# Performance work log

Measured on AMD Instinct MI355X. Metric: run time of the kernel, lower is better.

## Reference

```python
import jax, jax.numpy as jnp
import numpy as np

NEG_SLOPE = 0.2
BN_EPS = 1e-5

def gat_conv(x, src, dst, W, a_src, a_dst, bias, heads, out_ch):
    """PyG-style GATConv (eval mode, self-loops already in src/dst)."""
    N = x.shape[0]
    h = (x @ W).reshape(N, heads, out_ch)                 # [N,H,C]
    alpha_src = jnp.sum(h * a_src, axis=-1)               # [N,H]
    alpha_dst = jnp.sum(h * a_dst, axis=-1)               # [N,H]
    e = jax.nn.leaky_relu(alpha_src[src] + alpha_dst[dst], NEG_SLOPE)  # [E,H]
    # softmax over edges grouped by destination node
    m = jax.ops.segment_max(e, dst, num_segments=N)
    e = jnp.exp(e - m[dst])
    denom = jax.ops.segment_sum(e, dst, num_segments=N)
    alpha = e / (denom[dst] + 1e-16)                      # [E,H]
    msg = h[src] * alpha[:, :, None]                      # [E,H,C]
    out = jax.ops.segment_sum(msg, dst, num_segments=N)   # [N,H,C]
    return out.reshape(N, heads * out_ch) + bias

def bn_inf(x, gamma, beta, mean, var):
    return (x - mean) * jax.lax.rsqrt(var + BN_EPS) * gamma + beta

def setup_inputs() -> dict:
    key = jax.random.key(0)
    ks = iter(jax.random.split(key, 64))
    N, E, G = 50000, 800000, 256
    IN, H, HEADS, OUT = 58, 64, 4, 128
    D = H * HEADS  # 256
    inp = {}
    inp['x'] = jax.random.normal(next(ks), (N, IN), dtype=jnp.float32)
    inp['edge_index'] = jax.random.randint(next(ks), (2, E), 0, N)
    inp['batch'] = jnp.sort(jax.random.randint(next(ks), (N,), 0, G))
    inp['global_features'] = jax.random.normal(next(ks), (G, 7), dtype=jnp.float32)
    def lin(k, fi, fo):
        return jax.random.normal(k, (fi, fo), dtype=jnp.float32) / np.sqrt(fi)
    dims = [(IN, H, HEADS), (D, H, HEADS), (D, H, HEADS), (D, OUT, 1)]
    for i, (fi, c, hd) in enumerate(dims, 1):
        inp[f'W{i}'] = lin(next(ks), fi, hd * c)
        inp[f'a{i}s'] = jax.random.normal(next(ks), (hd, c), dtype=jnp.float32) / np.sqrt(c)
        inp[f'a{i}d'] = jax.random.normal(next(ks), (hd, c), dtype=jnp.float32) / np.sqrt(c)
        inp[f'b{i}'] = jnp.zeros((hd * c,), dtype=jnp.float32)
        bd = hd * c
        inp[f'g{i}'] = jnp.ones((bd,), dtype=jnp.float32)
        inp[f'be{i}'] = jnp.zeros((bd,), dtype=jnp.float32)
        inp[f'm{i}'] = 0.1 * jax.random.normal(next(ks), (bd,), dtype=jnp.float32)
        inp[f'v{i}'] = jax.random.uniform(next(ks), (bd,), dtype=jnp.float32) + 0.5
    inp['pw1'] = lin(next(ks), OUT, 32); inp['pb1'] = jnp.zeros((32,), jnp.float32)
    inp['pw2'] = lin(next(ks), 32, 1);   inp['pb2'] = jnp.zeros((1,), jnp.float32)
    inp['gw'] = lin(next(ks), 7, 32);    inp['gb'] = jnp.zeros((32,), jnp.float32)
    return inp

def reference(x, edge_index, batch, global_features,
              W1, a1s, a1d, b1, g1, be1, m1, v1,
              W2, a2s, a2d, b2, g2, be2, m2, v2,
              W3, a3s, a3d, b3, g3, be3, m3, v3,
              W4, a4s, a4d, b4, g4, be4, m4, v4,
              pw1, pb1, pw2, pb2, gw, gb):
    N = x.shape[0]
    G = global_features.shape[0]
    loops = jnp.arange(N)
    src = jnp.concatenate([edge_index[0], loops])  # add self-loops (PyG default)
    dst = jnp.concatenate([edge_index[1], loops])
    x1 = jax.nn.relu(bn_inf(gat_conv(x,  src, dst, W1, a1s, a1d, b1, 4, 64), g1, be1, m1, v1))
    x2 = jax.nn.relu(bn_inf(gat_conv(x1, src, dst, W2, a2s, a2d, b2, 4, 64), g2, be2, m2, v2))
    x3 = jax.nn.relu(bn_inf(gat_conv(x1 + x2, src, dst, W3, a3s, a3d, b3, 4, 64), g3, be3, m3, v3))
    x4 = jax.nn.relu(bn_inf(gat_conv(x3, src, dst, W4, a4s, a4d, b4, 1, 128), g4, be4, m4, v4))
    # GlobalAttention pooling: gate -> per-graph softmax -> weighted sum
    gate = jax.nn.relu(x4 @ pw1 + pb1) @ pw2 + pb2        # [N,1]
    gm = jax.ops.segment_max(gate, batch, num_segments=G)
    ge = jnp.exp(gate - gm[batch])
    gden = jax.ops.segment_sum(ge, batch, num_segments=G)
    attn = ge / (gden[batch] + 1e-16)                     # [N,1]
    emb = jax.ops.segment_sum(attn * x4, batch, num_segments=G)  # [G,128]
    gf = jax.nn.relu(global_features @ gw + gb)           # [G,32] (dropout off in eval)
    return jnp.concatenate([emb, gf], axis=-1)            # [G,160]
```

## Files before the change

kernel.cpp:

```cpp
#include <hip/hip_runtime.h>
#include <cstdint>
#include <cstddef>

#define NEG_SLOPE 0.2f
#define BN_EPS 1e-5f

typedef __bf16 bf16x8 __attribute__((ext_vector_type(8)));
typedef float  f32x4  __attribute__((ext_vector_type(4)));

__device__ __forceinline__ float ub0(unsigned u) { return (float)(u & 0xffu); }
__device__ __forceinline__ float ub1(unsigned u) { return (float)((u >> 8) & 0xffu); }
__device__ __forceinline__ float ub2(unsigned u) { return (float)((u >> 16) & 0xffu); }
__device__ __forceinline__ float ub3(unsigned u) { return (float)((u >> 24) & 0xffu); }

__global__ void conv_pad_kernel(const float* __restrict__ x, __bf16* __restrict__ xb,
                                int N, int K) {
    int i = blockIdx.x * blockDim.x + threadIdx.x;
    int total = N * 8;
    for (; i < total; i += gridDim.x * blockDim.x) {
        int n = i >> 3, p = i & 7;
        bf16x8 v;
        #pragma unroll
        for (int j = 0; j < 8; ++j) {
            int k = p * 8 + j;
            v[j] = (k < K) ? (__bf16)x[(size_t)n * K + k] : (__bf16)0.f;
        }
        *(bf16x8*)&xb[((size_t)p * N + n) * 8] = v;
    }
}

__global__ void prep_all_kernel(
    const float* __restrict__ W1, const float* __restrict__ W2,
    const float* __restrict__ W3, const float* __restrict__ W4,
    const float* __restrict__ PW1,
    __bf16* __restrict__ wt1, __bf16* __restrict__ wt2,
    __bf16* __restrict__ wt3, __bf16* __restrict__ wt4,
    __bf16* __restrict__ pw1t,
    const float* b1, const float* g1, const float* e1, const float* m1, const float* v1,
    const float* b2, const float* g2, const float* e2, const float* m2, const float* v2,
    const float* b3, const float* g3, const float* e3, const float* m3, const float* v3,
    const float* b4, const float* g4, const float* e4, const float* m4, const float* v4,
    float* __restrict__ bnS, float* __restrict__ bnT,
    int IN) {
    int b = blockIdx.x;
    if (b >= 928) {
        int l = b - 928;
        int Dl = (l == 3) ? 128 : 256;
        int t = threadIdx.x;
        if (t < Dl) {
            const float* bias; const float* ga; const float* be;
            const float* mu;   const float* va;
            if (l == 0)      { bias = b1; ga = g1; be = e1; mu = m1; va = v1; }
            else if (l == 1) { bias = b2; ga = g2; be = e2; mu = m2; va = v2; }
            else if (l == 2) { bias = b3; ga = g3; be = e3; mu = m3; va = v3; }
            else             { bias = b4; ga = g4; be = e4; mu = m4; va = v4; }
            float S = ga[t] * rsqrtf(va[t] + BN_EPS);
            bnS[l * 256 + t] = S;
            bnT[l * 256 + t] = (bias[t] - mu[t]) * S + be[t];
        }
        return;
    }
    const float* W; __bf16* WT; int K, D, Kpad, col; bool panel = true;
    if (b < 256)      { W = W1;  WT = wt1;  K = IN;  D = 256; Kpad = 64;  col = b; }
    else if (b < 512) { W = W2;  WT = wt2;  K = 256; D = 256; Kpad = 256; col = b - 256; }
    else if (b < 768) { W = W3;  WT = wt3;  K = 256; D = 256; Kpad = 256; col = b - 512; }
    else if (b < 896) { W = W4;  WT = wt4;  K = 256; D = 128; Kpad = 256; col = b - 768; }
    else              { W = PW1; WT = pw1t; K = 128; D = 32;  Kpad = 128; col = b - 896; panel = false; }
    for (int k = threadIdx.x; k < Kpad; k += blockDim.x) {
        float v = (k < K) ? W[(size_t)k * D + col] : 0.f;
        if (panel)
            WT[((size_t)(k >> 3) * D + col) * 8 + (k & 7)] = (__bf16)v;
        else
            WT[(size_t)col * Kpad + k] = (__bf16)v;
    }
}

template<int DCOLS, int KT, bool HAS_A2>
__global__ __launch_bounds__(256) void gemm_fused(
    const __bf16* __restrict__ A, const __bf16* __restrict__ A2,
    const __bf16* __restrict__ WT,
    const float* __restrict__ asv, const float* __restrict__ adv,
    uint8_t* __restrict__ H8, float* __restrict__ hscale,
    float* __restrict__ alpha_s, float* __restrict__ alpha_d,
    int M) {
    constexpr int NSB = DCOLS / 64;
    constexpr int RB  = (DCOLS == 256) ? 32 : 64;
    const int w    = threadIdx.x >> 6;
    const int lane = threadIdx.x & 63;
    const int l16  = lane & 15, hi4 = lane >> 4;
    const int rbase = (DCOLS == 256) ? 0 : (w >> 1) * 32;
    const int ct    = (DCOLS == 256) ? w : (w & 1);
    const int col0w = ct * 64;
    const int n0 = blockIdx.x * RB;

    f32x4 acc[2][4] = {};
    int arow[2];
    #pragma unroll
    for (int i = 0; i < 2; ++i) {
        int r = n0 + rbase + i * 16 + l16;
        arow[i] = (r < M) ? r : (M - 1);
    }

    #pragma unroll
    for (int k0 = 0; k0 < KT; k0 += 32) {
        const int panel = (k0 >> 3) + hi4;
        bf16x8 af[2], bfr[4];
        #pragma unroll
        for (int i = 0; i < 2; ++i) {
            bf16x8 v = *(const bf16x8*)&A[((size_t)panel * M + arow[i]) * 8];
            if (HAS_A2) {
                bf16x8 v2 = *(const bf16x8*)&A2[((size_t)panel * M + arow[i]) * 8];
                #pragma unroll
                for (int j = 0; j < 8; ++j) v[j] = (__bf16)((float)v[j] + (float)v2[j]);
            }
            af[i] = v;
        }
        #pragma unroll
        for (int j = 0; j < 4; ++j)
            bfr[j] = *(const bf16x8*)&WT[((size_t)panel * DCOLS + col0w + j * 16 + l16) * 8];
        #pragma unroll
        for (int i = 0; i < 2; ++i)
            #pragma unroll
            for (int j = 0; j < 4; ++j)
                acc[i][j] = __builtin_amdgcn_mfma_f32_16x16x32_bf16(
                    af[i], bfr[j], acc[i][j], 0, 0, 0);
    }

    float asc[4], adc[4];
    #pragma unroll
    for (int j = 0; j < 4; ++j) {
        int c = col0w + j * 16 + l16;
        asc[j] = asv[c]; adc[j] = adv[c];
    }
    __shared__ float as_l[(DCOLS == 128) ? 64 : 1][2], ad_l[(DCOLS == 128) ? 64 : 1][2];
    #pragma unroll
    for (int i = 0; i < 2; ++i)
        #pragma unroll
        for (int q = 0; q < 4; ++q) {
            float ps = 0.f, pd = 0.f;
            #pragma unroll
            for (int j = 0; j < 4; ++j) {
                float v = acc[i][j][q];
                ps = fmaf(v, asc[j], ps);
                pd = fmaf(v, adc[j], pd);
            }
            #pragma unroll
            for (int o = 1; o < 16; o <<= 1) {
                ps += __shfl_xor(ps, o, 64);
                pd += __shfl_xor(pd, o, 64);
            }
            int rl = rbase + i * 16 + hi4 * 4 + q;
            if constexpr (DCOLS == 256) {
                int row = n0 + rl;
                if (l16 == 0 && row < M) {
                    alpha_s[row * 4 + w] = ps;
                    alpha_d[row * 4 + w] = pd;
                }
            } else {
                if (l16 == 0) { as_l[rl][ct] = ps; ad_l[rl][ct] = pd; }
            }
        }
    if constexpr (DCOLS == 128) {
        __syncthreads();
        int t = threadIdx.x;
        if (t < 64) {
            int row = n0 + t;
            if (row < M) {
                alpha_s[row] = as_l[t][0] + as_l[t][1];
                alpha_d[row] = ad_l[t][0] + ad_l[t][1];
            }
        }
    }

    #pragma unroll
    for (int i = 0; i < 2; ++i)
        #pragma unroll
        for (int q = 0; q < 4; ++q) {
            float m = fabsf(acc[i][0][q]);
            #pragma unroll
            for (int j = 1; j < 4; ++j) m = fmaxf(m, fabsf(acc[i][j][q]));
            #pragma unroll
            for (int o = 1; o < 16; o <<= 1) m = fmaxf(m, __shfl_xor(m, o, 64));
            float qinv = (m > 1e-30f) ? 127.f / m : 0.f;
            int row = n0 + rbase + i * 16 + hi4 * 4 + q;
            if (row < M) {
                if (l16 == 0) hscale[row * NSB + ct] = m * (1.f / 127.f);
                #pragma unroll
                for (int j = 0; j < 4; ++j)
                    H8[(size_t)row * DCOLS + col0w + j * 16 + l16] =
                        (uint8_t)((int)rintf(acc[i][j][q] * qinv) + 128);
            }
        }
}

__global__ void deg_count_kernel(const int* __restrict__ ei, int* __restrict__ deg,
                                 int E, int Etot) {
    int e = blockIdx.x * blockDim.x + threadIdx.x;
    if (e >= Etot) return;
    int d = (e < E) ? ei[E + e] : e - E;
    atomicAdd(&deg[d], 1);
}

#define SCB 4096
__global__ __launch_bounds__(256) void scan1_kernel(const int* __restrict__ deg,
                                                    int* __restrict__ bsum, int N) {
    __shared__ int ts[256];
    const int t = threadIdx.x;
    const int base = blockIdx.x * SCB + t * 16;
    int s = 0;
    #pragma unroll
    for (int i = 0; i < 16; ++i) {
        int idx = base + i;
        if (idx < N) s += deg[idx];
    }
    ts[t] = s;
    __syncthreads();
    for (int off = 128; off > 0; off >>= 1) {
        if (t < off) ts[t] += ts[t + off];
        __syncthreads();
    }
    if (t == 0) bsum[blockIdx.x] = ts[0];
}

__global__ __launch_bounds__(256) void scan2_kernel(const int* __restrict__ bsum,
                                                    int* __restrict__ bpref, int B,
                                                    int* __restrict__ rowptrN) {
    __shared__ int sm[256];
    const int t = threadIdx.x;
    int v = (t < B) ? bsum[t] : 0;
    sm[t] = v;
    __syncthreads();
    for (int off = 1; off < 256; off <<= 1) {
        int u = (t >= off) ? sm[t - off] : 0;
        __syncthreads();
        sm[t] += u;
        __syncthreads();
    }
    if (t < B) bpref[t] = sm[t] - v;
    if (t == 255) *rowptrN = sm[255];
}

__global__ __launch_bounds__(256) void scan3_kernel(const int* __restrict__ deg,
                                                    const int* __restrict__ bpref,
                                                    int* __restrict__ rowptr,
                                                    int* __restrict__ cursor, int N) {
    __shared__ int ts[256];
    const int t = threadIdx.x;
    const int base = blockIdx.x * SCB + t * 16;
    int d[16];
    int s = 0;
    #pragma unroll
    for (int i = 0; i < 16; ++i) {
        int idx = base + i;
        d[i] = (idx < N) ? deg[idx] : 0;
        s += d[i];
    }
    ts[t] = s;
    __syncthreads();
    for (int off = 1; off < 256; off <<= 1) {
        int u = (t >= off) ? ts[t - off] : 0;
        __syncthreads();
        ts[t] += u;
        __syncthreads();
    }
    int run = bpref[blockIdx.x] + ts[t] - s;
    #pragma unroll
    for (int i = 0; i < 16; ++i) {
        int idx = base + i;
        if (idx < N) { rowptr[idx] = run; cursor[idx] = run; run += d[i]; }
    }
}

__global__ void scatter_kernel(const int* __restrict__ ei, int* __restrict__ cursor,
                               int* __restrict__ csrc, int E, int Etot) {
    int e = blockIdx.x * blockDim.x + threadIdx.x;
    if (e >= Etot) return;
    int s, d;
    if (e < E) { s = ei[e]; d = ei[E + e]; } else { s = d = e - E; }
    int pos = atomicAdd(&cursor[d], 1);
    csrc[pos] = s;
}

__global__ void gstart_kernel(const int* __restrict__ batch, int* __restrict__ gstart,
                              int N, int G) {
    int n = blockIdx.x * blockDim.x + threadIdx.x;
    if (n >= N) return;
    int b = batch[n];
    if (n == 0) { for (int g = 0; g <= b; ++g) gstart[g] = 0; }
    else {
        int bp = batch[n - 1];
        for (int g = bp + 1; g <= b; ++g) gstart[g] = n;
    }
    if (n == N - 1) { for (int g = b + 1; g <= G; ++g) gstart[g] = N; }
}

template<int HEADS, int C, bool OUTP>
__global__ __launch_bounds__(256) void gat_agg(
    const int* __restrict__ rowptr, const int* __restrict__ csrc,
    const uint8_t* __restrict__ hf, const float* __restrict__ hscale,
    const float* __restrict__ asrc, const float* __restrict__ adst,
    const float* __restrict__ bnS, const float* __restrict__ bnT,
    __bf16* __restrict__ out, int N) {
    constexpr int D   = HEADS * C;
    constexpr int NSB = D / 64;
    constexpr int LPE = D / 8;
    constexpr int EPH = 32 / LPE;

    const int wid  = threadIdx.x >> 6;
    const int lane = threadIdx.x & 63;
    const int half = lane >> 5;
    const int sl   = lane & 31;

    __shared__ int   soff[4][2][32];
    __shared__ float pal[4][2][32][NSB];

    const int npairs = (N + 1) >> 1;

    for (int pair = blockIdx.x * 4 + wid; pair < npairs; pair += gridDim.x * 4) {
        const int node = pair * 2 + half;
        const bool valid = node < N;
        const int beg = valid ? rowptr[node] : 0;
        const int end = valid ? rowptr[node + 1] : 0;
        const int deg = end - beg;

        const int grp = (EPH == 1) ? 0 : (sl >> 4);
        const int c0  = (EPH == 1) ? sl * 8 : (sl & 15) * 8;
        const int sb  = c0 >> 6;
        const uint8_t* hb = hf + c0;

        float ad[HEADS];
        #pragma unroll
        for (int h = 0; h < HEADS; ++h) ad[h] = valid ? adst[node * HEADS + h] : 0.f;

        float acc8[8] = {};
        float psum = 0.f;

        auto fmau8 = [&](uint2 v, float q) {
            acc8[0] = fmaf(ub0(v.x), q, acc8[0]);
            acc8[1] = fmaf(ub1(v.x), q, acc8[1]);
            acc8[2] = fmaf(ub2(v.x), q, acc8[2]);
            acc8[3] = fmaf(ub3(v.x), q, acc8[3]);
            acc8[4] = fmaf(ub0(v.y), q, acc8[4]);
            acc8[5] = fmaf(ub1(v.y), q, acc8[5]);
            acc8[6] = fmaf(ub2(v.y), q, acc8[6]);
            acc8[7] = fmaf(ub3(v.y), q, acc8[7]);
        };

        auto agg_chunk = [&](int cnt) {
            const int steps = (cnt + 8 * EPH - 1) / (8 * EPH);
            for (int s = 0; s < steps; ++s) {
                const int e = s * 8 * EPH;
                int o[8]; float q[8]; uint2 v[8];
                #pragma unroll
                for (int u = 0; u < 8; ++u) {
                    o[u] = soff[wid][half][e + u * EPH + grp];
                    q[u] = pal[wid][half][e + u * EPH + grp][sb];
                }
                #pragma unroll
                for (int u = 0; u < 8; ++u) v[u] = *(const uint2*)(hb + o[u]);
                #pragma unroll
                for (int u = 0; u < 8; ++u) { psum += q[u]; fmau8(v[u], q[u]); }
            }
        };

        if (deg <= 32) {
            const bool act = sl < deg;
            int msrc = act ? csrc[beg + sl] : 0;
            float lv[HEADS];
            if constexpr (HEADS == 4) {
                float4 a4 = ((const float4*)asrc)[msrc];
                lv[0] = a4.x; lv[1] = a4.y; lv[2] = a4.z; lv[3] = a4.w;
            } else {
                lv[0] = asrc[msrc];
            }
            float pe_[HEADS];
            #pragma unroll
            for (int h = 0; h < HEADS; ++h) {
                float v;
                if (act) { v = lv[h] + ad[h]; v = v > 0.f ? v : NEG_SLOPE * v; }
                else v = -INFINITY;
                float mx = v;
                #pragma unroll
                for (int o = 1; o < 32; o <<= 1) mx = fmaxf(mx, __shfl_xor(mx, o, 64));
                float pe = act ? __expf(v - mx) : 0.f;
                float ps = pe;
                #pragma unroll
                for (int o = 1; o < 32; o <<= 1) ps += __shfl_xor(ps, o, 64);
                pe_[h] = pe * (1.f / (ps + 1e-16f));
            }
            soff[wid][half][sl] = msrc * D;
            if constexpr (HEADS == 4) {
                float4 hs = act ? ((const float4*)hscale)[msrc]
                                : make_float4(0.f, 0.f, 0.f, 0.f);
                *(float4*)&pal[wid][half][sl][0] =
                    make_float4(pe_[0] * hs.x, pe_[1] * hs.y, pe_[2] * hs.z, pe_[3] * hs.w);
            } else {
                float2 hs = act ? ((const float2*)hscale)[msrc] : make_float2(0.f, 0.f);
                *(float2*)&pal[wid][half][sl][0] = make_float2(pe_[0] * hs.x, pe_[0] * hs.y);
            }
            asm volatile("s_waitcnt lgkmcnt(0)" ::: "memory");
            agg_chunk(deg);
        } else {
            float mx[HEADS], sm[HEADS], inv[HEADS];
            #pragma unroll
            for (int h = 0; h < HEADS; ++h) mx[h] = -INFINITY;
            for (int j = beg + sl; j < end; j += 32) {
                int s = csrc[j];
                #pragma unroll
                for (int h = 0; h < HEADS; ++h) {
                    float v = asrc[s * HEADS + h] + ad[h];
                    v = v > 0.f ? v : NEG_SLOPE * v;
                    mx[h] = fmaxf(mx[h], v);
                }
            }
            #pragma unroll
            for (int h = 0; h < HEADS; ++h) {
                #pragma unroll
                for (int o = 1; o < 32; o <<= 1) mx[h] = fmaxf(mx[h], __shfl_xor(mx[h], o, 64));
                sm[h] = 0.f;
            }
            for (int j = beg + sl; j < end; j += 32) {
                int s = csrc[j];
                #pragma unroll
                for (int h = 0; h < HEADS; ++h) {
                    float v = asrc[s * HEADS + h] + ad[h];
                    v = v > 0.f ? v : NEG_SLOPE * v;
                    sm[h] += __expf(v - mx[h]);
                }
            }
            #pragma unroll
            for (int h = 0; h < HEADS; ++h) {
                #pragma unroll
                for (int o = 1; o < 32; o <<= 1) sm[h] += __shfl_xor(sm[h], o, 64);
                inv[h] = 1.f / (sm[h] + 1e-16f);
            }
            for (int base2 = beg; base2 < end; base2 += 32) {
                int ne = min(32, end - base2);
                bool act2 = sl < ne;
                int msrc = csrc[base2 + (act2 ? sl : 0)];
                soff[wid][half][sl] = msrc * D;
                if constexpr (HEADS == 4) {
                    float4 hs = act2 ? ((const float4*)hscale)[msrc]
                                     : make_float4(0.f, 0.f, 0.f, 0.f);
                    float hsv[4] = {hs.x, hs.y, hs.z, hs.w};
                    #pragma unroll
                    for (int h = 0; h < 4; ++h) {
                        float pv = 0.f;
                        if (act2) {
                            float v = asrc[msrc * 4 + h] + ad[h];
                            v = v > 0.f ? v : NEG_SLOPE * v;
                            pv = __expf(v - mx[h]) * inv[h];
                        }
                        pal[wid][half][sl][h] = pv * hsv[h];
                    }
                } else {
                    float2 hs = act2 ? ((const float2*)hscale)[msrc] : make_float2(0.f, 0.f);
                    float pv = 0.f;
                    if (act2) {
                        float v = asrc[msrc] + ad[0];
                        v = v > 0.f ? v : NEG_SLOPE * v;
                        pv = __expf(v - mx[0]) * inv[0];
                    }
                    pal[wid][half][sl][0] = pv * hs.x;
                    pal[wid][half][sl][1] = pv * hs.y;
                }
                asm volatile("s_waitcnt lgkmcnt(0)" ::: "memory");
                agg_chunk(ne);
                asm volatile("s_waitcnt lgkmcnt(0)" ::: "memory");
            }
        }

        if constexpr (EPH == 2) {
            #pragma unroll
            for (int i = 0; i < 8; ++i)
                acc8[i] += __shfl_xor(acc8[i], 16, 64);
            psum += __shfl_xor(psum, 16, 64);
        }

        if (valid && (EPH == 1 || sl < 16)) {
            float4 Sa = *(const float4*)&bnS[c0];
            float4 Sb = *(const float4*)&bnS[c0 + 4];
            float4 Ta = *(const float4*)&bnT[c0];
            float4 Tb = *(const float4*)&bnT[c0 + 4];
            float S8[8] = {Sa.x, Sa.y, Sa.z, Sa.w, Sb.x, Sb.y, Sb.z, Sb.w};
            float T8[8] = {Ta.x, Ta.y, Ta.z, Ta.w, Tb.x, Tb.y, Tb.z, Tb.w};
            bf16x8 ov;
            #pragma unroll
            for (int i = 0; i < 8; ++i) {
                float v = fmaf(acc8[i] - 128.f * psum, S8[i], T8[i]);
                ov[i] = (__bf16)fmaxf(v, 0.f);
            }
            if constexpr (OUTP)
                *(bf16x8*)&out[((size_t)(c0 >> 3) * N + node) * 8] = ov;
            else
                *(bf16x8*)&out[(size_t)node * D + c0] = ov;
        }
    }
}

__global__ __launch_bounds__(256) void gate_gemm_kernel(
    const __bf16* __restrict__ x4, const __bf16* __restrict__ pw1t,
    const float* __restrict__ pb1, const float* __restrict__ pw2,
    const float* __restrict__ pb2, float* __restrict__ gate, int N) {
    const int w    = threadIdx.x >> 6;
    const int lane = threadIdx.x & 63;
    const int l16  = lane & 15, hi4 = lane >> 4;
    const int n0 = (blockIdx.x * 4 + w) * 16;
    if (n0 >= N) return;
    const int arow = min(n0 + l16, N - 1);
    f32x4 acc[2] = {};
    #pragma unroll
    for (int k0 = 0; k0 < 128; k0 += 32) {
        bf16x8 af = *(const bf16x8*)&x4[(size_t)arow * 128 + k0 + hi4 * 8];
        bf16x8 b0 = *(const bf16x8*)&pw1t[(size_t)l16 * 128 + k0 + hi4 * 8];
        bf16x8 b1 = *(const bf16x8*)&pw1t[(size_t)(16 + l16) * 128 + k0 + hi4 * 8];
        acc[0] = __builtin_amdgcn_mfma_f32_16x16x32_bf16(af, b0, acc[0], 0, 0, 0);
        acc[1] = __builtin_amdgcn_mfma_f32_16x16x32_bf16(af, b1, acc[1], 0, 0, 0);
    }
    float pb1a = pb1[l16], pb1b = pb1[16 + l16];
    float w2a = pw2[l16], w2b = pw2[16 + l16];
    #pragma unroll
    for (int q = 0; q < 4; ++q) {
        float g = fmaxf(acc[0][q] + pb1a, 0.f) * w2a +
                  fmaxf(acc[1][q] + pb1b, 0.f) * w2b;
        #pragma unroll
        for (int o = 1; o < 16; o <<= 1) g += __shfl_xor(g, o, 64);
        int row = n0 + hi4 * 4 + q;
        if (l16 == 0 && row < N) gate[row] = g + pb2[0];
    }
}

__global__ __launch_bounds__(128) void pool_kernel(
    const __bf16* __restrict__ x4, const float* __restrict__ gate,
    const int* __restrict__ gstart, float* __restrict__ out) {
    const int g = blockIdx.x;
    const int t = threadIdx.x;
    const int beg = gstart[g], end = gstart[g + 1];
    __shared__ float red[128];
    __shared__ float wbuf[128];
    float m = -INFINITY;
    for (int n = beg + t; n < end; n += 128) m = fmaxf(m, gate[n]);
    red[t] = m; __syncthreads();
    for (int off = 64; off > 0; off >>= 1) {
        if (t < off) red[t] = fmaxf(red[t], red[t + off]);
        __syncthreads();
    }
    m = red[0]; __syncthreads();
    float s = 0.f;
    for (int n = beg + t; n < end; n += 128) s += expf(gate[n] - m);
    red[t] = s; __syncthreads();
    for (int off = 64; off > 0; off >>= 1) {
        if (t < off) red[t] += red[t + off];
        __syncthreads();
    }
    const float inv = 1.f / (red[0] + 1e-16f);
    __syncthreads();
    float acc = 0.f;
    for (int base = beg; base < end; base += 128) {
        int ne = min(128, end - base);
        if (t < ne) wbuf[t] = expf(gate[base + t] - m) * inv;
        __syncthreads();
        for (int i = 0; i < ne; ++i)
            acc = fmaf(wbuf[i], (float)x4[(size_t)(base + i) * 128 + t], acc);
        __syncthreads();
    }
    out[(size_t)g * 160 + t] = acc;
}

__global__ void gfeat_kernel(const float* __restrict__ gfeat,
                             const float* __restrict__ gw, const float* __restrict__ gb,
                             float* __restrict__ out) {
    const int g = blockIdx.x;
    const int k = threadIdx.x;
    if (k < 32) {
        float t = gb[k];
        #pragma unroll
        for (int j = 0; j < 7; ++j) t = fmaf(gfeat[g * 7 + j], gw[j * 32 + k], t);
        out[(size_t)g * 160 + 128 + k] = fmaxf(t, 0.f);
    }
}

extern "C" void kernel_launch(void* const* d_in, const int* in_sizes, int n_in,
                              void* d_out, int out_size, void* d_ws, size_t ws_size,
                              hipStream_t stream) {
    const float* x      = (const float*)d_in[0];
    const int*   ei     = (const int*)  d_in[1];
    const int*   batch  = (const int*)  d_in[2];
    const float* gfeat  = (const float*)d_in[3];

    const int N    = in_sizes[2];
    const int E    = in_sizes[1] / 2;
    const int G    = in_sizes[3] / 7;
    const int IN   = in_sizes[0] / N;
    const int Etot = E + N;

    const float* W[4];  const float* avs[4]; const float* avd[4]; const float* bi[4];
    const float* ga[4]; const float* be[4];  const float* mu[4];  const float* va[4];
    for (int l = 0; l < 4; ++l) {
        int o = 4 + 8 * l;
        W[l]   = (const float*)d_in[o + 0];
        avs[l] = (const float*)d_in[o + 1];
        avd[l] = (const float*)d_in[o + 2];
        bi[l]  = (const float*)d_in[o + 3];
        ga[l]  = (const float*)d_in[o + 4];
        be[l]  = (const float*)d_in[o + 5];
        mu[l]  = (const float*)d_in[o + 6];
        va[l]  = (const float*)d_in[o + 7];
    }
    const float* pw1 = (const float*)d_in[36];
    const float* pb1 = (const float*)d_in[37];
    const float* pw2 = (const float*)d_in[38];
    const float* pb2 = (const float*)d_in[39];
    const float* gw  = (const float*)d_in[40];
    const float* gb  = (const float*)d_in[41];

    float* out = (float*)d_out;

    float* ws = (float*)d_ws;
    __bf16* xb = (__bf16*)ws; ws += (size_t)N * 32;
    uint8_t* h8 = (uint8_t*)ws; ws += (size_t)N * 64;
    float* hsc = ws;  ws += (size_t)N * 4;
    __bf16* x1 = (__bf16*)ws; ws += (size_t)N * 128;
    __bf16* x2 = (__bf16*)ws; ws += (size_t)N * 128;
    __bf16* x3 = (__bf16*)ws; ws += (size_t)N * 128;
    __bf16* wt1 = (__bf16*)ws; ws += 256 * 64 / 2;
    __bf16* wt2 = (__bf16*)ws; ws += 256 * 256 / 2;
    __bf16* wt3 = (__bf16*)ws; ws += 256 * 256 / 2;
    __bf16* wt4 = (__bf16*)ws; ws += 128 * 256 / 2;
    __bf16* pw1t = (__bf16*)ws; ws += 32 * 128 / 2;
    float* bnS = ws; ws += 4 * 256;
    float* bnT = ws; ws += 4 * 256;
    float* asrc = ws;  ws += (size_t)N * 4;
    float* adst = ws;  ws += (size_t)N * 4;
    float* gate = ws;  ws += N;
    int* deg    = (int*)ws; ws += N;
    int* cursor = (int*)ws; ws += N;
    int* rowptr = (int*)ws; ws += (N + 1);
    int* csrc   = (int*)ws; ws += Etot;
    int* gstart = (int*)ws; ws += (G + 1);
    int* bsum   = (int*)ws; ws += 256;
    int* bpref  = (int*)ws; ws += 256;
    __bf16* x4 = x1;

    const int SB = (N + SCB - 1) / SCB;

    hipLaunchKernelGGL(conv_pad_kernel, dim3(512), dim3(256), 0, stream, x, xb, N, IN);
    hipLaunchKernelGGL(prep_all_kernel, dim3(932), dim3(256), 0, stream,
                       W[0], W[1], W[2], W[3], pw1, wt1, wt2, wt3, wt4, pw1t,
                       bi[0], ga[0], be[0], mu[0], va[0],
                       bi[1], ga[1], be[1], mu[1], va[1],
                       bi[2], ga[2], be[2], mu[2], va[2],
                       bi[3], ga[3], be[3], mu[3], va[3],
                       bnS, bnT, IN);

    hipMemsetAsync(deg, 0, (size_t)N * 4, stream);
    hipLaunchKernelGGL(deg_count_kernel, dim3((Etot + 255) / 256), dim3(256), 0, stream,
                       ei, deg, E, Etot);
    hipLaunchKernelGGL(scan1_kernel, dim3(SB), dim3(256), 0, stream, deg, bsum, N);
    hipLaunchKernelGGL(scan2_kernel, dim3(1), dim3(256), 0, stream, bsum, bpref, SB,
                       &rowptr[N]);
    hipLaunchKernelGGL(scan3_kernel, dim3(SB), dim3(256), 0, stream, deg, bpref,
                       rowptr, cursor, N);
    hipLaunchKernelGGL(scatter_kernel, dim3((Etot + 255) / 256), dim3(256), 0, stream,
                       ei, cursor, csrc, E, Etot);
    hipLaunchKernelGGL(gstart_kernel, dim3((N + 255) / 256), dim3(256), 0, stream,
                       batch, gstart, N, G);

    const int grid32  = (N + 31) / 32;
    const int grid64  = (N + 63) / 64;
    const int gatgrid = 2048;

    hipLaunchKernelGGL((gemm_fused<256, 64, false>), dim3(grid32), dim3(256), 0, stream,
                       xb, nullptr, wt1, avs[0], avd[0], h8, hsc, asrc, adst, N);
    hipLaunchKernelGGL((gat_agg<4, 64, true>), dim3(gatgrid), dim3(256), 0, stream,
                       rowptr, csrc, h8, hsc, asrc, adst, bnS + 0, bnT + 0, x1, N);
    hipLaunchKernelGGL((gemm_fused<256, 256, false>), dim3(grid32), dim3(256), 0, stream,
                       x1, nullptr, wt2, avs[1], avd[1], h8, hsc, asrc, adst, N);
    hipLaunchKernelGGL((gat_agg<4, 64, true>), dim3(gatgrid), dim3(256), 0, stream,
                       rowptr, csrc, h8, hsc, asrc, adst, bnS + 256, bnT + 256, x2, N);
    hipLaunchKernelGGL((gemm_fused<256, 256, true>), dim3(grid32), dim3(256), 0, stream,
                       x1, x2, wt3, avs[2], avd[2], h8, hsc, asrc, adst, N);
    hipLaunchKernelGGL((gat_agg<4, 64, true>), dim3(gatgrid), dim3(256), 0, stream,
                       rowptr, csrc, h8, hsc, asrc, adst, bnS + 512, bnT + 512, x3, N);
    hipLaunchKernelGGL((gemm_fused<128, 256, false>), dim3(grid64), dim3(256), 0, stream,
                       x3, nullptr, wt4, avs[3], avd[3], h8, hsc, asrc, adst, N);
    hipLaunchKernelGGL((gat_agg<1, 128, false>), dim3(gatgrid), dim3(256), 0, stream,
                       rowptr, csrc, h8, hsc, asrc, adst, bnS + 768, bnT + 768, x4, N);

    hipLaunchKernelGGL(gate_gemm_kernel, dim3((N + 63) / 64), dim3(256), 0, stream,
                       x4, pw1t, pb1, pw2, pb2, gate, N);
    hipLaunchKernelGGL(pool_kernel, dim3(G), dim3(128), 0, stream, x4, gate, gstart, out);
    hipLaunchKernelGGL(gfeat_kernel, dim3(G), dim3(64), 0, stream, gfeat, gw, gb, out);
}
```

Measured before the change: 410.5 us.

## Build CSR via two-level bucket partition instead of global atomic scatter

Replaces the per-node degree count, three-pass scan and global-atomic scatter with a bucketed counting sort. Edges are first counted and partitioned into buckets of 128 destination nodes using shared-memory atomics, then each bucket is sorted locally in LDS to produce rowptr and csrc. This aims to cut contended global atomics and scattered writes during CSR construction, at the cost of an extra temporary int2 edge buffer and one more pass over the edges. It assumes at most 512 buckets, so N must not exceed 65536.

```diff
diff --git a/kernel.cpp b/kernel.cpp
--- a/kernel.cpp
+++ b/kernel.cpp
@@ -193,92 +193,123 @@
         }
 }
 
-__global__ void deg_count_kernel(const int* __restrict__ ei, int* __restrict__ deg,
-                                 int E, int Etot) {
-    int e = blockIdx.x * blockDim.x + threadIdx.x;
-    if (e >= Etot) return;
-    int d = (e < E) ? ei[E + e] : e - E;
-    atomicAdd(&deg[d], 1);
-}
-
-#define SCB 4096
-__global__ __launch_bounds__(256) void scan1_kernel(const int* __restrict__ deg,
-                                                    int* __restrict__ bsum, int N) {
-    __shared__ int ts[256];
+#define NPB_SHIFT 7
+#define NPB 128
+#define NBMAX 512
+#define P3CH 4096
+#define STAGE 4608
+
+__global__ __launch_bounds__(256) void bcount_kernel(const int* __restrict__ ei,
+                                                     int* __restrict__ bcnt,
+                                                     int E, int Etot) {
+    __shared__ int bc[NBMAX];
+    for (int i = threadIdx.x; i < NBMAX; i += 256) bc[i] = 0;
+    __syncthreads();
+    for (int e = blockIdx.x * blockDim.x + threadIdx.x; e < Etot;
+         e += gridDim.x * blockDim.x) {
+        int d = (e < E) ? ei[E + e] : e - E;
+        atomicAdd(&bc[d >> NPB_SHIFT], 1);
+    }
+    __syncthreads();
+    for (int i = threadIdx.x; i < NBMAX; i += 256)
+        if (bc[i]) atomicAdd(&bcnt[i], bc[i]);
+}
+
+__global__ __launch_bounds__(512) void bscan_kernel(const int* __restrict__ bcnt,
+                                                    int* __restrict__ bbase,
+                                                    int* __restrict__ bcursor,
+                                                    int* __restrict__ rowptrN, int Etot) {
+    __shared__ int sm[512];
     const int t = threadIdx.x;
-    const int base = blockIdx.x * SCB + t * 16;
-    int s = 0;
-    #pragma unroll
-    for (int i = 0; i < 16; ++i) {
-        int idx = base + i;
-        if (idx < N) s += deg[idx];
-    }
-    ts[t] = s;
-    __syncthreads();
-    for (int off = 128; off > 0; off >>= 1) {
-        if (t < off) ts[t] += ts[t + off];
-        __syncthreads();
-    }
-    if (t == 0) bsum[blockIdx.x] = ts[0];
-}
-
-__global__ __launch_bounds__(256) void scan2_kernel(const int* __restrict__ bsum,
-                                                    int* __restrict__ bpref, int B,
-                                                    int* __restrict__ rowptrN) {
-    __shared__ int sm[256];
+    int v = bcnt[t];
+    sm[t] = v;
+    __syncthreads();
+    for (int off = 1; off < 512; off <<= 1) {
+        int u = (t >= off) ? sm[t - off] : 0;
+        __syncthreads();
+        sm[t] += u;
+        __syncthreads();
+    }
+    bbase[t] = sm[t] - v;
+    bcursor[t] = sm[t] - v;
+    if (t == 0) *rowptrN = Etot;
+}
+
+__global__ __launch_bounds__(256) void partition_kernel(const int* __restrict__ ei,
+                                                        int* __restrict__ bcursor,
+                                                        int2* __restrict__ tmp,
+                                                        int E, int Etot) {
+    __shared__ int lcnt[NBMAX], gb[NBMAX], lcur[NBMAX];
     const int t = threadIdx.x;
-    int v = (t < B) ? bsum[t] : 0;
-    sm[t] = v;
-    __syncthreads();
-    for (int off = 1; off < 256; off <<= 1) {
-        int u = (t >= off) ? sm[t - off] : 0;
-        __syncthreads();
-        sm[t] += u;
-        __syncthreads();
-    }
-    if (t < B) bpref[t] = sm[t] - v;
-    if (t == 255) *rowptrN = sm[255];
-}
-
-__global__ __launch_bounds__(256) void scan3_kernel(const int* __restrict__ deg,
-                                                    const int* __restrict__ bpref,
-                                                    int* __restrict__ rowptr,
-                                                    int* __restrict__ cursor, int N) {
-    __shared__ int ts[256];
+    const int base = blockIdx.x * P3CH;
+    for (int i = t; i < NBMAX; i += 256) { lcnt[i] = 0; lcur[i] = 0; }
+    __syncthreads();
+    for (int i = t; i < P3CH; i += 256) {
+        int e = base + i;
+        if (e < Etot) {
+            int d = (e < E) ? ei[E + e] : e - E;
+            atomicAdd(&lcnt[d >> NPB_SHIFT], 1);
+        }
+    }
+    __syncthreads();
+    for (int i = t; i < NBMAX; i += 256)
+        if (lcnt[i] > 0) gb[i] = atomicAdd(&bcursor[i], lcnt[i]);
+    __syncthreads();
+    for (int i = t; i < P3CH; i += 256) {
+        int e = base + i;
+        if (e < Etot) {
+            int s, d;
+            if (e < E) { s = ei[e]; d = ei[E + e]; } else { s = d = e - E; }
+            int b = d >> NPB_SHIFT;
+            int pos = gb[b] + atomicAdd(&lcur[b], 1);
+            tmp[pos] = make_int2(s, d);
+        }
+    }
+}
+
+__global__ __launch_bounds__(256) void bucket_build_kernel(
+    const int2* __restrict__ tmp, const int* __restrict__ bbase,
+    const int* __restrict__ bcnt,
+    int* __restrict__ rowptr, int* __restrict__ csrc, int N) {
+    __shared__ int ncnt[NPB];
+    __shared__ int nst[NPB];
+    __shared__ int stage[STAGE];
+    const int b = blockIdx.x;
     const int t = threadIdx.x;
-    const int base = blockIdx.x * SCB + t * 16;
-    int d[16];
-    int s = 0;
-    #pragma unroll
-    for (int i = 0; i < 16; ++i) {
-        int idx = base + i;
-        d[i] = (idx < N) ? deg[idx] : 0;
-        s += d[i];
-    }
-    ts[t] = s;
-    __syncthreads();
-    for (int off = 1; off < 256; off <<= 1) {
-        int u = (t >= off) ? ts[t - off] : 0;
-        __syncthreads();
-        ts[t] += u;
-        __syncthreads();
-    }
-    int run = bpref[blockIdx.x] + ts[t] - s;
-    #pragma unroll
-    for (int i = 0; i < 16; ++i) {
-        int idx = base + i;
-        if (idx < N) { rowptr[idx] = run; cursor[idx] = run; run += d[i]; }
-    }
-}
-
-__global__ void scatter_kernel(const int* __restrict__ ei, int* __restrict__ cursor,
-                               int* __restrict__ csrc, int E, int Etot) {
-    int e = blockIdx.x * blockDim.x + threadIdx.x;
-    if (e >= Etot) return;
-    int s, d;
-    if (e < E) { s = ei[e]; d = ei[E + e]; } else { s = d = e - E; }
-    int pos = atomicAdd(&cursor[d], 1);
-    csrc[pos] = s;
+    const int node0 = b << NPB_SHIFT;
+    const int nn = min(NPB, N - node0);
+    const int pbase = bbase[b];
+    const int cnt = bcnt[b];
+    const bool fits = (cnt <= STAGE);
+    for (int i = t; i < NPB; i += 256) ncnt[i] = 0;
+    __syncthreads();
+    for (int i = t; i < cnt; i += 256) {
+        int2 p = tmp[pbase + i];
+        atomicAdd(&ncnt[p.y - node0], 1);
+    }
+    __syncthreads();
+    if (t < NPB) nst[t] = ncnt[t];
+    __syncthreads();
+    for (int off = 1; off < NPB; off <<= 1) {
+        int u = (t < NPB && t >= off) ? nst[t - off] : 0;
+        __syncthreads();
+        if (t < NPB) nst[t] += u;
+        __syncthreads();
+    }
+    if (t < nn) rowptr[node0 + t] = pbase + nst[t] - ncnt[t];
+    __syncthreads();
+    if (t < NPB) ncnt[t] = nst[t] - ncnt[t];
+    __syncthreads();
+    for (int i = t; i < cnt; i += 256) {
+        int2 p = tmp[pbase + i];
+        int lpos = atomicAdd(&ncnt[p.y - node0], 1);
+        if (fits) stage[lpos] = p.x;
+        else      csrc[pbase + lpos] = p.x;
+    }
+    __syncthreads();
+    if (fits)
+        for (int i = t; i < cnt; i += 256)
+            csrc[pbase + i] = stage[i];
 }
 
 __global__ void gstart_kernel(const int* __restrict__ batch, int* __restrict__ gstart,
@@ -633,16 +664,17 @@
     float* asrc = ws;  ws += (size_t)N * 4;
     float* adst = ws;  ws += (size_t)N * 4;
     float* gate = ws;  ws += N;
-    int* deg    = (int*)ws; ws += N;
-    int* cursor = (int*)ws; ws += N;
     int* rowptr = (int*)ws; ws += (N + 1);
     int* csrc   = (int*)ws; ws += Etot;
     int* gstart = (int*)ws; ws += (G + 1);
-    int* bsum   = (int*)ws; ws += 256;
-    int* bpref  = (int*)ws; ws += 256;
+    int* bcnt   = (int*)ws; ws += NBMAX;
+    int* bbase  = (int*)ws; ws += NBMAX;
+    int* bcursor= (int*)ws; ws += NBMAX;
+    ws = (float*)(((uintptr_t)ws + 15) & ~(uintptr_t)15);
+    int2* tmp   = (int2*)ws; ws += (size_t)Etot * 2;
     __bf16* x4 = x1;
 
-    const int SB = (N + SCB - 1) / SCB;
+    const int NB = (N + NPB - 1) / NPB;
 
     hipLaunchKernelGGL(conv_pad_kernel, dim3(512), dim3(256), 0, stream, x, xb, N, IN);
     hipLaunchKernelGGL(prep_all_kernel, dim3(932), dim3(256), 0, stream,
@@ -653,16 +685,14 @@
                        bi[3], ga[3], be[3], mu[3], va[3],
                        bnS, bnT, IN);
 
-    hipMemsetAsync(deg, 0, (size_t)N * 4, stream);
-    hipLaunchKernelGGL(deg_count_kernel, dim3((Etot + 255) / 256), dim3(256), 0, stream,
-                       ei, deg, E, Etot);
-    hipLaunchKernelGGL(scan1_kernel, dim3(SB), dim3(256), 0, stream, deg, bsum, N);
-    hipLaunchKernelGGL(scan2_kernel, dim3(1), dim3(256), 0, stream, bsum, bpref, SB,
-                       &rowptr[N]);
-    hipLaunchKernelGGL(scan3_kernel, dim3(SB), dim3(256), 0, stream, deg, bpref,
-                       rowptr, cursor, N);
-    hipLaunchKernelGGL(scatter_kernel, dim3((Etot + 255) / 256), dim3(256), 0, stream,
-                       ei, cursor, csrc, E, Etot);
+    hipMemsetAsync(bcnt, 0, NBMAX * sizeof(int), stream);
+    hipLaunchKernelGGL(bcount_kernel, dim3(256), dim3(256), 0, stream, ei, bcnt, E, Etot);
+    hipLaunchKernelGGL(bscan_kernel, dim3(1), dim3(512), 0, stream,
+                       bcnt, bbase, bcursor, &rowptr[N], Etot);
+    hipLaunchKernelGGL(partition_kernel, dim3((Etot + P3CH - 1) / P3CH), dim3(256), 0,
+                       stream, ei, bcursor, tmp, E, Etot);
+    hipLaunchKernelGGL(bucket_build_kernel, dim3(NB), dim3(256), 0, stream,
+                       tmp, bbase, bcnt, rowptr, csrc, N);
     hipLaunchKernelGGL(gstart_kernel, dim3((N + 255) / 256), dim3(256), 0, stream,
                        batch, gstart, N, G);
 
```

New measurement: 351.0 us. 14.5% less time.
